# Performance work log

Measured on AMD Instinct MI355X. Metric: run time of the kernel, lower is better.

Reference implementation:

```python
import jax, jax.numpy as jnp
import numpy as np

E = 8          # num_experts
K = 2          # top_k
ALPHA = 0.01   # aux_loss_coef


def setup_inputs() -> dict:
    key = jax.random.key(0)
    k1, k2, k3, k4 = jax.random.split(key, 4)
    x = jax.random.normal(k1, (4, 4096, 768), jnp.float32)
    gate_w = jax.random.normal(k2, (E, 768), jnp.float32) * 0.02   # Router gate [E, H]
    w1 = jax.random.normal(k3, (E, 3072, 768), jnp.float32) * 0.02  # per-expert [I, H]
    w2 = jax.random.normal(k4, (E, 768, 3072), jnp.float32) * 0.02  # per-expert [H, I]
    return {"x": x, "gate_w": gate_w, "w1": w1, "w2": w2}


def reference(x, gate_w, w1, w2):
    B, S, H = x.shape
    N = B * S
    x_flat = x.reshape(N, H)

    # ---- Router: top-K gating ----
    gate_logits = x_flat @ gate_w.T                      # [N, E]
    gate_probs = jax.nn.softmax(gate_logits, axis=-1)    # [N, E]
    top_weights, top_indices = jax.lax.top_k(gate_probs, K)  # [N, K] each
    top_weights = top_weights / top_weights.sum(-1, keepdims=True)

    # ---- Load balancing aux loss ----
    counts = jnp.zeros(E, gate_probs.dtype).at[top_indices.reshape(-1)].add(1.0)
    f = counts / (N * K)
    p = gate_probs.mean(axis=0)
    aux_loss = ALPHA * E * jnp.sum(f * p)

    # ---- Dispatch + per-expert FFN + weighted combine ----
    # combine[n, e] = sum_k top_weights[n, k] * [top_indices[n, k] == e]
    combine = jnp.zeros((N, E), x_flat.dtype).at[
        jnp.arange(N)[:, None], top_indices
    ].add(top_weights)                                   # [N, E]

    y = jnp.zeros_like(x_flat)
    for e in range(E):  # fixed small loop over experts
        h = jax.nn.gelu(x_flat @ w1[e].T, approximate=True)  # [N, I] (GELU-tanh)
        y = y + combine[:, e:e + 1] * (h @ w2[e].T)          # [N, H]

    return y.reshape(B, S, H), aux_loss
```

## Files before the change

kernel.cpp:

```cpp
#include <hip/hip_runtime.h>
#include <hip/hip_bf16.h>

#define N_TOK 16384
#define H_DIM 768
#define I_DIM 3072
#define NEXP 8
#define RBLK 1024

typedef short bf16x8 __attribute__((ext_vector_type(8)));
typedef float f32x4 __attribute__((ext_vector_type(4)));

__device__ __forceinline__ unsigned short f2bf(float f) {
    unsigned int u = __float_as_uint(f);
    u += 0x7fffu + ((u >> 16) & 1u);
    return (unsigned short)(u >> 16);
}

__device__ __forceinline__ float gelu_tanh(float v) {
    float u = 0.7978845608028654f * (v + 0.044715f * v * v * v);
    float t = __expf(2.0f * fminf(u, 15.0f));
    return 0.5f * v * (1.0f + (t - 1.0f) / (t + 1.0f));
}

__device__ __forceinline__ void gll16(const void* g, void* l) {
    __builtin_amdgcn_global_load_lds(
        (const __attribute__((address_space(1))) unsigned int*)g,
        (__attribute__((address_space(3))) unsigned int*)l, 16, 0, 0);
}

__global__ __launch_bounds__(256) void moe_router(
    const float* __restrict__ x, const float* __restrict__ gw,
    unsigned short* __restrict__ xbf,
    int* __restrict__ topidx, float* __restrict__ topw,
    float* __restrict__ partials)
{
    __shared__ float gws[NEXP * H_DIM];
    __shared__ float red[64];
    const int tid = threadIdx.x;
    for (int i = tid * 4; i < NEXP * H_DIM; i += 1024)
        *(float4*)(gws + i) = *(const float4*)(gw + i);
    __syncthreads();

    const int lane = tid & 63;
    const int wid = tid >> 6;
    const int tbase = blockIdx.x * 16 + wid * 4;

    float lcnt[8], lps[8];
#pragma unroll
    for (int e = 0; e < 8; ++e) { lcnt[e] = 0.f; lps[e] = 0.f; }

#pragma unroll
    for (int k = 0; k < 4; ++k) {
        const int t = tbase + k;
        float acc[8] = {0.f, 0.f, 0.f, 0.f, 0.f, 0.f, 0.f, 0.f};
#pragma unroll
        for (int j = 0; j < 3; ++j) {
            const int col = j * 256 + lane * 4;
            float4 xv = *(const float4*)(x + (size_t)t * H_DIM + col);
            ushort4 o;
            o.x = f2bf(xv.x); o.y = f2bf(xv.y); o.z = f2bf(xv.z); o.w = f2bf(xv.w);
            *(ushort4*)(xbf + (size_t)t * H_DIM + col) = o;
#pragma unroll
            for (int e = 0; e < 8; ++e) {
                float4 g = *(const float4*)(gws + e * H_DIM + col);
                acc[e] += xv.x * g.x + xv.y * g.y + xv.z * g.z + xv.w * g.w;
            }
        }
#pragma unroll
        for (int off = 32; off >= 1; off >>= 1)
#pragma unroll
            for (int e = 0; e < 8; ++e) acc[e] += __shfl_xor(acc[e], off, 64);

        int e0 = 0;
#pragma unroll
        for (int e = 1; e < 8; ++e) if (acc[e] > acc[e0]) e0 = e;
        int e1 = (e0 == 0) ? 1 : 0;
#pragma unroll
        for (int e = 0; e < 8; ++e) if (e != e0 && acc[e] > acc[e1]) e1 = e;

        float mx = acc[0];
#pragma unroll
        for (int e = 1; e < 8; ++e) mx = fmaxf(mx, acc[e]);
        float p[8]; float s = 0.f;
#pragma unroll
        for (int e = 0; e < 8; ++e) { p[e] = expf(acc[e] - mx); s += p[e]; }
        float inv = 1.0f / s;
#pragma unroll
        for (int e = 0; e < 8; ++e) p[e] *= inv;

        float wsum = p[e0] + p[e1];
        if (lane == 0) {
            topidx[2 * t] = e0; topidx[2 * t + 1] = e1;
            topw[2 * t] = p[e0] / wsum; topw[2 * t + 1] = p[e1] / wsum;
            lcnt[e0] += 1.f; lcnt[e1] += 1.f;
#pragma unroll
            for (int e = 0; e < 8; ++e) lps[e] += p[e];
        }
    }

    if (lane == 0) {
#pragma unroll
        for (int e = 0; e < 8; ++e) {
            red[wid * 16 + e] = lcnt[e];
            red[wid * 16 + 8 + e] = lps[e];
        }
    }
    __syncthreads();
    if (tid < 16)
        partials[blockIdx.x * 16 + tid] =
            red[tid] + red[16 + tid] + red[32 + tid] + red[48 + tid];
}

__global__ __launch_bounds__(256) void moe_rank(
    const int* __restrict__ topidx, const float* __restrict__ topw,
    const float* __restrict__ partials, int* __restrict__ offs,
    float* __restrict__ aux_out, int* __restrict__ perm, float* __restrict__ pw)
{
    const int b = blockIdx.x;
    const int tid = threadIdx.x;
    __shared__ float stot[256], spre[256];
    __shared__ float tot[16];
    __shared__ int pfx[8];

    const int c = tid & 15;
    float vtot = 0.f, vpre = 0.f;
    for (int r = tid >> 4; r < RBLK; r += 16) {
        float v = partials[r * 16 + c];
        vtot += v;
        if (r < b) vpre += v;
    }
    stot[tid] = vtot; spre[tid] = vpre;
    __syncthreads();
    if (tid < 16) {
        float t = 0.f, q = 0.f;
#pragma unroll
        for (int k = 0; k < 16; ++k) { t += stot[k * 16 + tid]; q += spre[k * 16 + tid]; }
        tot[tid] = t;
        if (tid < 8) spre[tid] = q;
    }
    __syncthreads();
    if (tid == 0) {
        int run = 0;
        float aux = 0.f;
#pragma unroll
        for (int e = 0; e < 8; ++e) {
            pfx[e] = run + (int)(spre[e] + 0.5f);
            aux += (tot[e] / (float)(N_TOK * 2)) * (tot[8 + e] / (float)N_TOK);
            if (b == 0) offs[e] = run;
            run += (int)(tot[e] + 0.5f);
        }
        if (b == 0) { offs[8] = run; *aux_out = 0.01f * 8.0f * aux; }
    }
    __syncthreads();
    if (tid < 32) {
        const int t = b * 16 + (tid >> 1);
        const int slot = tid & 1;
        const int myexp = topidx[2 * t + slot];
        int rank = 0;
#pragma unroll
        for (int ee = 0; ee < 8; ++ee) {
            unsigned long long m = __ballot(myexp == ee);
            if (myexp == ee)
                rank = pfx[ee] + __popcll(m & ((1ull << tid) - 1ull));
        }
        perm[rank] = t;
        pw[rank] = topw[2 * t + slot];
    }
}

__global__ __launch_bounds__(256) void moe_cvt2(
    const float* __restrict__ a, unsigned short* __restrict__ oa,
    const float* __restrict__ bsrc, unsigned short* __restrict__ ob, int n)
{
    int idx = (blockIdx.x * 256 + threadIdx.x) * 4;
    const int stride = gridDim.x * 1024;
    for (; idx < 2 * n; idx += stride) {
        const float* in = (idx < n) ? a : bsrc;
        unsigned short* out = (idx < n) ? oa : ob;
        const int i = (idx < n) ? idx : idx - n;
        float4 v = *(const float4*)(in + i);
        ushort4 o;
        o.x = f2bf(v.x); o.y = f2bf(v.y); o.z = f2bf(v.z); o.w = f2bf(v.w);
        *(ushort4*)(out + i) = o;
    }
}


#define GEMM_STAGE(t)                                                             \
    { const int s_ = (t) & 3;                                                     \
      gll16(asrc0 + (t) * 32, As + s_ * 4096 +        tid * 8);                   \
      gll16(asrc1 + (t) * 32, As + s_ * 4096 + 2048 + tid * 8);                   \
      gll16(bsrc0 + (t) * 32, Bs + s_ * 4096 +        tid * 8);                   \
      gll16(bsrc1 + (t) * 32, Bs + s_ * 4096 + 2048 + tid * 8); }

#define GEMM_LOADFRAG(t)                                                          \
      const unsigned short* Ab_ = As + ((t) & 3) * 4096 + rowbase + pA * 8;       \
      const unsigned short* Bb_ = Bs + ((t) & 3) * 4096 + rowbase + pB * 8;       \
      bf16x8 a_[4], b_[4];                                                        \
      _Pragma("unroll")                                                           \
      for (int i_ = 0; i_ < 4; ++i_) a_[i_] = *(const bf16x8*)(Ab_ + i_ * 1024);  \
      _Pragma("unroll")                                                           \
      for (int j_ = 0; j_ < 4; ++j_) b_[j_] = *(const bf16x8*)(Bb_ + j_ * 1024);

#define GEMM_MFMA()                                                               \
      __builtin_amdgcn_s_setprio(1);                                              \
      _Pragma("unroll")                                                           \
      for (int i_ = 0; i_ < 4; ++i_)                                              \
      _Pragma("unroll")                                                           \
      for (int j_ = 0; j_ < 4; ++j_)                                              \
          acc[i_][j_] = __builtin_amdgcn_mfma_f32_16x16x32_bf16(                  \
              a_[i_], b_[j_], acc[i_][j_], 0, 0, 0);                              \
      __builtin_amdgcn_s_setprio(0);

#define GEMM_SYNC(N_IMM)                                                          \
    asm volatile("s_waitcnt vmcnt(" #N_IMM ")" ::: "memory");                     \
    __builtin_amdgcn_s_barrier();                                                 \
    __builtin_amdgcn_sched_barrier(0);

#define GEMM_PIPELINE(NT)                                                         \
    GEMM_STAGE(0); GEMM_STAGE(1); GEMM_STAGE(2);                                  \
    GEMM_SYNC(8);                                                                 \
    for (int t = 0; t < (NT) - 3; ++t) {                                          \
        GEMM_LOADFRAG(t);                                                         \
        GEMM_STAGE(t + 3);                                                        \
        GEMM_MFMA();                                                              \
        GEMM_SYNC(8);                                                             \
    }                                                                             \
    { GEMM_LOADFRAG((NT) - 3); GEMM_MFMA(); }                                     \
    GEMM_SYNC(4);                                                                 \
    { GEMM_LOADFRAG((NT) - 2); GEMM_MFMA(); }                                     \
    GEMM_SYNC(0);                                                                 \
    { GEMM_LOADFRAG((NT) - 1); GEMM_MFMA(); }

__global__ __launch_bounds__(256) void moe_gemm1(
    const unsigned short* __restrict__ xbf,
    const unsigned short* __restrict__ w1bf,
    const int* __restrict__ perm, const int* __restrict__ offs,
    unsigned short* __restrict__ hbuf, int e0)
{
    const int e = e0 + blockIdx.z;
    const int off = offs[e];
    const int n_e = offs[e + 1] - off;
    const int rt = blockIdx.y;
    if (rt * 128 >= n_e) return;
    const int ct = blockIdx.x;
    const int coff = off - offs[e0];

    __shared__ __align__(16) unsigned short As[4 * 4096];
    __shared__ __align__(16) unsigned short Bs[4 * 4096];

    const int tid = threadIdx.x;
    const int lane = tid & 63;
    const int wid = tid >> 6;
    const int wr = wid >> 1, wc = wid & 1;

    const int m = tid >> 3;
    const int csw = (tid & 7) ^ (m & 7);
    const int hi = csw >> 2, kc = csw & 3;

    const unsigned short* asrc0; const unsigned short* asrc1;
    const unsigned short* bsrc0; const unsigned short* bsrc1;
    {
        int g0 = hi * 64 + m, g1 = hi * 64 + 32 + m;
        int lr0 = rt * 128 + g0; if (lr0 >= n_e) lr0 = n_e - 1;
        int lr1 = rt * 128 + g1; if (lr1 >= n_e) lr1 = n_e - 1;
        asrc0 = xbf + (size_t)perm[off + lr0] * H_DIM + kc * 8;
        asrc1 = xbf + (size_t)perm[off + lr1] * H_DIM + kc * 8;
        bsrc0 = w1bf + ((size_t)e * I_DIM + ct * 128 + g0) * H_DIM + kc * 8;
        bsrc1 = w1bf + ((size_t)e * I_DIM + ct * 128 + g1) * H_DIM + kc * 8;
    }

    const int pA = ((wr << 2) | (lane >> 4)) ^ (lane & 7);
    const int pB = ((wc << 2) | (lane >> 4)) ^ (lane & 7);
    const int rowbase = (lane & 15) * 64;

    f32x4 acc[4][4] = {};

    GEMM_PIPELINE(H_DIM / 32);

    const int rbase = rt * 128 + wr * 64 + (lane >> 4) * 4;
    const int cbase = ct * 128 + wc * 64 + (lane & 15);
#pragma unroll
    for (int i = 0; i < 4; ++i) {
#pragma unroll
        for (int r = 0; r < 4; ++r) {
            const int lr = rbase + i * 16 + r;
            if (lr < n_e) {
                unsigned short* dst = hbuf + (size_t)(coff + lr) * I_DIM + cbase;
#pragma unroll
                for (int j = 0; j < 4; ++j)
                    dst[j * 16] = f2bf(gelu_tanh(acc[i][j][r]));
            }
        }
    }
}

__global__ __launch_bounds__(256) void moe_gemm2(
    const unsigned short* __restrict__ hbuf,
    const unsigned short* __restrict__ w2bf,
    const int* __restrict__ perm, const float* __restrict__ pw,
    const int* __restrict__ offs, float* __restrict__ y, int e0)
{
    const int e = e0 + blockIdx.z;
    const int off = offs[e];
    const int n_e = offs[e + 1] - off;
    const int rt = blockIdx.y;
    if (rt * 128 >= n_e) return;
    const int ct = blockIdx.x;
    const int coff = off - offs[e0];

    __shared__ __align__(16) unsigned short As[4 * 4096];
    __shared__ __align__(16) unsigned short Bs[4 * 4096];

    const int tid = threadIdx.x;
    const int lane = tid & 63;
    const int wid = tid >> 6;
    const int wr = wid >> 1, wc = wid & 1;

    const int m = tid >> 3;
    const int csw = (tid & 7) ^ (m & 7);
    const int hi = csw >> 2, kc = csw & 3;

    const unsigned short* asrc0; const unsigned short* asrc1;
    const unsigned short* bsrc0; const unsigned short* bsrc1;
    {
        int g0 = hi * 64 + m, g1 = hi * 64 + 32 + m;
        int lr0 = rt * 128 + g0; if (lr0 >= n_e) lr0 = n_e - 1;
        int lr1 = rt * 128 + g1; if (lr1 >= n_e) lr1 = n_e - 1;
        asrc0 = hbuf + (size_t)(coff + lr0) * I_DIM + kc * 8;
        asrc1 = hbuf + (size_t)(coff + lr1) * I_DIM + kc * 8;
        bsrc0 = w2bf + ((size_t)e * H_DIM + ct * 128 + g0) * I_DIM + kc * 8;
        bsrc1 = w2bf + ((size_t)e * H_DIM + ct * 128 + g1) * I_DIM + kc * 8;
    }

    const int pA = ((wr << 2) | (lane >> 4)) ^ (lane & 7);
    const int pB = ((wc << 2) | (lane >> 4)) ^ (lane & 7);
    const int rowbase = (lane & 15) * 64;

    f32x4 acc[4][4] = {};

    GEMM_PIPELINE(I_DIM / 32);

    const int rbase = rt * 128 + wr * 64 + (lane >> 4) * 4;
    const int cbase = ct * 128 + wc * 64 + (lane & 15);
#pragma unroll
    for (int i = 0; i < 4; ++i) {
#pragma unroll
        for (int r = 0; r < 4; ++r) {
            const int lr = rbase + i * 16 + r;
            if (lr < n_e) {
                const int token = perm[off + lr];
                const float w = pw[off + lr];
                float* dst = y + (size_t)token * H_DIM + cbase;
#pragma unroll
                for (int j = 0; j < 4; ++j)
                    atomicAdd(dst + j * 16, w * acc[i][j][r]);
            }
        }
    }
}

extern "C" void kernel_launch(void* const* d_in, const int* in_sizes, int n_in,
                              void* d_out, int out_size, void* d_ws, size_t ws_size,
                              hipStream_t stream) {
    const float* x  = (const float*)d_in[0];
    const float* gw = (const float*)d_in[1];
    const float* w1 = (const float*)d_in[2];
    const float* w2 = (const float*)d_in[3];
    float* y = (float*)d_out;

    char* base = (char*)d_ws;
    size_t o = 0;
    unsigned short* xbf  = (unsigned short*)(base + o); o += (size_t)N_TOK * H_DIM * 2;
    unsigned short* w1bf = (unsigned short*)(base + o); o += (size_t)NEXP * I_DIM * H_DIM * 2;
    unsigned short* w2bf = (unsigned short*)(base + o); o += (size_t)NEXP * H_DIM * I_DIM * 2;
    int*   topidx = (int*)(base + o);   o += (size_t)N_TOK * 2 * 4;
    float* topw   = (float*)(base + o); o += (size_t)N_TOK * 2 * 4;
    int*   perm   = (int*)(base + o);   o += (size_t)N_TOK * 2 * 4;
    float* pw     = (float*)(base + o); o += (size_t)N_TOK * 2 * 4;
    float* partials = (float*)(base + o); o += (size_t)RBLK * 16 * 4;
    int*   offs     = (int*)(base + o);   o += 64;
    unsigned short* hbuf = (unsigned short*)(base + o);
    size_t remain = (ws_size > o) ? (ws_size - o) : 0;

    long cap_rows = (long)(remain / (size_t)(I_DIM * 2));
    int nch;
    if (cap_rows >= 32768)      nch = 1;
    else if (cap_rows >= 18022) nch = 2;
    else if (cap_rows >= 9011)  nch = 4;
    else                        nch = 8;
    const int G = NEXP / nch;

    hipMemsetAsync(d_out, 0, (size_t)out_size * 4, stream);

    moe_router<<<RBLK, 256, 0, stream>>>(x, gw, xbf, topidx, topw, partials);
    moe_cvt2<<<4096, 256, 0, stream>>>(w1, w1bf, w2, w2bf, NEXP * I_DIM * H_DIM);
    moe_rank<<<RBLK, 256, 0, stream>>>(topidx, topw, partials, offs,
                                       y + (size_t)N_TOK * H_DIM, perm, pw);

    for (int c = 0; c < nch; ++c) {
        const int e0 = c * G;
        moe_gemm1<<<dim3(24, 128, G), 256, 0, stream>>>(
            xbf, w1bf, perm, offs, hbuf, e0);
        moe_gemm2<<<dim3(6, 128, G), 256, 0, stream>>>(
            hbuf, w2bf, perm, pw, offs, y, e0);
    }
}
```

Baseline: 678.6 us.

## Enlarge MoE GEMM tiles to 256x256 with 512-thread blocks

Both expert GEMM kernels move from 128x128 tiles with 4 waves to 256x256 tiles with 8 waves. Each wave now computes a 128x64 sub-tile with an 8x4 MFMA accumulator grid. The shared-memory staging buffers double to 64 KB per operand pair, and the grid shrinks to match. The goal is more arithmetic per byte loaded from global and LDS memory, at the cost of more registers, larger LDS use that limits occupancy, and more padding waste on partially filled expert row tiles.

```diff
diff --git a/kernel.cpp b/kernel.cpp
--- a/kernel.cpp
+++ b/kernel.cpp
@@ -188,24 +188,24 @@
 
 #define GEMM_STAGE(t)                                                             \
     { const int s_ = (t) & 3;                                                     \
-      gll16(asrc0 + (t) * 32, As + s_ * 4096 +        tid * 8);                   \
-      gll16(asrc1 + (t) * 32, As + s_ * 4096 + 2048 + tid * 8);                   \
-      gll16(bsrc0 + (t) * 32, Bs + s_ * 4096 +        tid * 8);                   \
-      gll16(bsrc1 + (t) * 32, Bs + s_ * 4096 + 2048 + tid * 8); }
+      gll16(asrc0 + (t) * 32, As + s_ * 8192 +        tid * 8);                   \
+      gll16(asrc1 + (t) * 32, As + s_ * 8192 + 4096 + tid * 8);                   \
+      gll16(bsrc0 + (t) * 32, Bs + s_ * 8192 +        tid * 8);                   \
+      gll16(bsrc1 + (t) * 32, Bs + s_ * 8192 + 4096 + tid * 8); }
 
 #define GEMM_LOADFRAG(t)                                                          \
-      const unsigned short* Ab_ = As + ((t) & 3) * 4096 + rowbase + pA * 8;       \
-      const unsigned short* Bb_ = Bs + ((t) & 3) * 4096 + rowbase + pB * 8;       \
-      bf16x8 a_[4], b_[4];                                                        \
+      const unsigned short* Ab_ = As + ((t) & 3) * 8192 + pAoff;                  \
+      const unsigned short* Bb_ = Bs + ((t) & 3) * 8192 + pBoff;                  \
+      bf16x8 a_[8], b_[4];                                                        \
       _Pragma("unroll")                                                           \
-      for (int i_ = 0; i_ < 4; ++i_) a_[i_] = *(const bf16x8*)(Ab_ + i_ * 1024);  \
+      for (int i_ = 0; i_ < 8; ++i_) a_[i_] = *(const bf16x8*)(Ab_ + i_ * 1024);  \
       _Pragma("unroll")                                                           \
       for (int j_ = 0; j_ < 4; ++j_) b_[j_] = *(const bf16x8*)(Bb_ + j_ * 1024);
 
 #define GEMM_MFMA()                                                               \
       __builtin_amdgcn_s_setprio(1);                                              \
       _Pragma("unroll")                                                           \
-      for (int i_ = 0; i_ < 4; ++i_)                                              \
+      for (int i_ = 0; i_ < 8; ++i_)                                              \
       _Pragma("unroll")                                                           \
       for (int j_ = 0; j_ < 4; ++j_)                                              \
           acc[i_][j_] = __builtin_amdgcn_mfma_f32_16x16x32_bf16(                  \
@@ -232,7 +232,7 @@
     GEMM_SYNC(0);                                                                 \
     { GEMM_LOADFRAG((NT) - 1); GEMM_MFMA(); }
 
-__global__ __launch_bounds__(256) void moe_gemm1(
+__global__ __launch_bounds__(512) void moe_gemm1(
     const unsigned short* __restrict__ xbf,
     const unsigned short* __restrict__ w1bf,
     const int* __restrict__ perm, const int* __restrict__ offs,
@@ -242,17 +242,17 @@
     const int off = offs[e];
     const int n_e = offs[e + 1] - off;
     const int rt = blockIdx.y;
-    if (rt * 128 >= n_e) return;
+    if (rt * 256 >= n_e) return;
     const int ct = blockIdx.x;
     const int coff = off - offs[e0];
 
-    __shared__ __align__(16) unsigned short As[4 * 4096];
-    __shared__ __align__(16) unsigned short Bs[4 * 4096];
+    __shared__ __align__(16) unsigned short As[4 * 8192];
+    __shared__ __align__(16) unsigned short Bs[4 * 8192];
 
     const int tid = threadIdx.x;
     const int lane = tid & 63;
     const int wid = tid >> 6;
-    const int wr = wid >> 1, wc = wid & 1;
+    const int wm = wid >> 2, wn = wid & 3;
 
     const int m = tid >> 3;
     const int csw = (tid & 7) ^ (m & 7);
@@ -261,27 +261,27 @@
     const unsigned short* asrc0; const unsigned short* asrc1;
     const unsigned short* bsrc0; const unsigned short* bsrc1;
     {
-        int g0 = hi * 64 + m, g1 = hi * 64 + 32 + m;
-        int lr0 = rt * 128 + g0; if (lr0 >= n_e) lr0 = n_e - 1;
-        int lr1 = rt * 128 + g1; if (lr1 >= n_e) lr1 = n_e - 1;
+        int r0 = hi * 128 + m, r1 = r0 + 64;
+        int lr0 = rt * 256 + r0; if (lr0 >= n_e) lr0 = n_e - 1;
+        int lr1 = rt * 256 + r1; if (lr1 >= n_e) lr1 = n_e - 1;
         asrc0 = xbf + (size_t)perm[off + lr0] * H_DIM + kc * 8;
         asrc1 = xbf + (size_t)perm[off + lr1] * H_DIM + kc * 8;
-        bsrc0 = w1bf + ((size_t)e * I_DIM + ct * 128 + g0) * H_DIM + kc * 8;
-        bsrc1 = w1bf + ((size_t)e * I_DIM + ct * 128 + g1) * H_DIM + kc * 8;
-    }
-
-    const int pA = ((wr << 2) | (lane >> 4)) ^ (lane & 7);
-    const int pB = ((wc << 2) | (lane >> 4)) ^ (lane & 7);
-    const int rowbase = (lane & 15) * 64;
-
-    f32x4 acc[4][4] = {};
+        bsrc0 = w1bf + ((size_t)e * I_DIM + ct * 256 + r0) * H_DIM + kc * 8;
+        bsrc1 = w1bf + ((size_t)e * I_DIM + ct * 256 + r1) * H_DIM + kc * 8;
+    }
+
+    const int pAoff = (lane & 15) * 64 + ((((wm << 2) | (lane >> 4)) ^ (lane & 7)) << 3);
+    const int pBoff = (wn & 1) * 4096 + (lane & 15) * 64 +
+                      (((((wn >> 1) << 2) | (lane >> 4)) ^ (lane & 7)) << 3);
+
+    f32x4 acc[8][4] = {};
 
     GEMM_PIPELINE(H_DIM / 32);
 
-    const int rbase = rt * 128 + wr * 64 + (lane >> 4) * 4;
-    const int cbase = ct * 128 + wc * 64 + (lane & 15);
-#pragma unroll
-    for (int i = 0; i < 4; ++i) {
+    const int rbase = rt * 256 + wm * 128 + (lane >> 4) * 4;
+    const int cbase = ct * 256 + wn * 64 + (lane & 15);
+#pragma unroll
+    for (int i = 0; i < 8; ++i) {
 #pragma unroll
         for (int r = 0; r < 4; ++r) {
             const int lr = rbase + i * 16 + r;
@@ -295,7 +295,7 @@
     }
 }
 
-__global__ __launch_bounds__(256) void moe_gemm2(
+__global__ __launch_bounds__(512) void moe_gemm2(
     const unsigned short* __restrict__ hbuf,
     const unsigned short* __restrict__ w2bf,
     const int* __restrict__ perm, const float* __restrict__ pw,
@@ -305,17 +305,17 @@
     const int off = offs[e];
     const int n_e = offs[e + 1] - off;
     const int rt = blockIdx.y;
-    if (rt * 128 >= n_e) return;
+    if (rt * 256 >= n_e) return;
     const int ct = blockIdx.x;
     const int coff = off - offs[e0];
 
-    __shared__ __align__(16) unsigned short As[4 * 4096];
-    __shared__ __align__(16) unsigned short Bs[4 * 4096];
+    __shared__ __align__(16) unsigned short As[4 * 8192];
+    __shared__ __align__(16) unsigned short Bs[4 * 8192];
 
     const int tid = threadIdx.x;
     const int lane = tid & 63;
     const int wid = tid >> 6;
-    const int wr = wid >> 1, wc = wid & 1;
+    const int wm = wid >> 2, wn = wid & 3;
 
     const int m = tid >> 3;
     const int csw = (tid & 7) ^ (m & 7);
@@ -324,27 +324,27 @@
     const unsigned short* asrc0; const unsigned short* asrc1;
     const unsigned short* bsrc0; const unsigned short* bsrc1;
     {
-        int g0 = hi * 64 + m, g1 = hi * 64 + 32 + m;
-        int lr0 = rt * 128 + g0; if (lr0 >= n_e) lr0 = n_e - 1;
-        int lr1 = rt * 128 + g1; if (lr1 >= n_e) lr1 = n_e - 1;
+        int r0 = hi * 128 + m, r1 = r0 + 64;
+        int lr0 = rt * 256 + r0; if (lr0 >= n_e) lr0 = n_e - 1;
+        int lr1 = rt * 256 + r1; if (lr1 >= n_e) lr1 = n_e - 1;
         asrc0 = hbuf + (size_t)(coff + lr0) * I_DIM + kc * 8;
         asrc1 = hbuf + (size_t)(coff + lr1) * I_DIM + kc * 8;
-        bsrc0 = w2bf + ((size_t)e * H_DIM + ct * 128 + g0) * I_DIM + kc * 8;
-        bsrc1 = w2bf + ((size_t)e * H_DIM + ct * 128 + g1) * I_DIM + kc * 8;
-    }
-
-    const int pA = ((wr << 2) | (lane >> 4)) ^ (lane & 7);
-    const int pB = ((wc << 2) | (lane >> 4)) ^ (lane & 7);
-    const int rowbase = (lane & 15) * 64;
-
-    f32x4 acc[4][4] = {};
+        bsrc0 = w2bf + ((size_t)e * H_DIM + ct * 256 + r0) * I_DIM + kc * 8;
+        bsrc1 = w2bf + ((size_t)e * H_DIM + ct * 256 + r1) * I_DIM + kc * 8;
+    }
+
+    const int pAoff = (lane & 15) * 64 + ((((wm << 2) | (lane >> 4)) ^ (lane & 7)) << 3);
+    const int pBoff = (wn & 1) * 4096 + (lane & 15) * 64 +
+                      (((((wn >> 1) << 2) | (lane >> 4)) ^ (lane & 7)) << 3);
+
+    f32x4 acc[8][4] = {};
 
     GEMM_PIPELINE(I_DIM / 32);
 
-    const int rbase = rt * 128 + wr * 64 + (lane >> 4) * 4;
-    const int cbase = ct * 128 + wc * 64 + (lane & 15);
-#pragma unroll
-    for (int i = 0; i < 4; ++i) {
+    const int rbase = rt * 256 + wm * 128 + (lane >> 4) * 4;
+    const int cbase = ct * 256 + wn * 64 + (lane & 15);
+#pragma unroll
+    for (int i = 0; i < 8; ++i) {
 #pragma unroll
         for (int r = 0; r < 4; ++r) {
             const int lr = rbase + i * 16 + r;
@@ -400,9 +400,9 @@
 
     for (int c = 0; c < nch; ++c) {
         const int e0 = c * G;
-        moe_gemm1<<<dim3(24, 128, G), 256, 0, stream>>>(
+        moe_gemm1<<<dim3(12, 64, G), 512, 0, stream>>>(
             xbf, w1bf, perm, offs, hbuf, e0);
-        moe_gemm2<<<dim3(6, 128, G), 256, 0, stream>>>(
+        moe_gemm2<<<dim3(3, 64, G), 512, 0, stream>>>(
             hbuf, w2bf, perm, pw, offs, y, e0);
     }
 }
```

After: 602.7 us (median of 4 runs). 11.2% less time.
